# Kernel tuning notes

Hardware: AMD Instinct MI355X
Metric: run time of the kernel (lower is better)

The kernel has to match this reference:

```python
import jax, jax.numpy as jnp
import numpy as np
from jax import lax

V = 10475
J = 55
B = 512
# Kinematic tree: hardcoded chain (parent[i] = i-1), root = 0.
PARENTS = np.concatenate([[-1], np.arange(J - 1)]).astype(np.int32)


def rodrigues(r):
    """Axis-angle (..., 3) -> rotation matrices (..., 3, 3)."""
    angle = jnp.sqrt(jnp.sum(r * r, axis=-1, keepdims=True) + 1e-12)  # (...,1)
    axis = r / angle
    s = jnp.sin(angle)[..., None]
    c = jnp.cos(angle)[..., None]
    kx, ky, kz = axis[..., 0], axis[..., 1], axis[..., 2]
    z = jnp.zeros_like(kx)
    K = jnp.stack([z, -kz, ky, kz, z, -kx, -ky, kx, z], axis=-1).reshape(r.shape[:-1] + (3, 3))
    I = jnp.eye(3, dtype=r.dtype)
    return I + s * K + (1.0 - c) * (K @ K)


def setup_inputs() -> dict:
    key = jax.random.key(0)
    ks = jax.random.split(key, 16)
    inp = {
        'shape': jax.random.normal(ks[0], (1, 10), jnp.float32),
        'body_pose': jax.random.normal(ks[1], (B, 21, 3), jnp.float32) * 0.3,
        'hand_pose': jax.random.normal(ks[2], (B, 30, 3), jnp.float32) * 0.3,
        'head_pose': jax.random.normal(ks[3], (B, 3, 3), jnp.float32) * 0.3,
        'expression': jax.random.normal(ks[4], (B, 10), jnp.float32),
        'pelvis_rotation': jax.random.normal(ks[5], (B, 3), jnp.float32) * 0.3,
        'global_translation': jax.random.normal(ks[6], (B, 3), jnp.float32),
        'v_template': jax.random.normal(ks[7], (V, 3), jnp.float32),
        'shapedirs': jax.random.normal(ks[8], (V, 3, 10), jnp.float32) * 0.01,
        'exprdirs': jax.random.normal(ks[9], (V, 3, 10), jnp.float32) * 0.01,
        'posedirs': jax.random.normal(ks[10], (486, V * 3), jnp.float32) * 0.001,
    }
    w = jax.random.uniform(ks[11], (V, J), jnp.float32)
    inp['lbs_weights'] = w / jnp.sum(w, axis=-1, keepdims=True)
    jr = jax.random.uniform(ks[12], (J, V), jnp.float32)
    inp['J_regressor'] = jr / jnp.sum(jr, axis=-1, keepdims=True)
    inp['hand_mean'] = jax.random.normal(ks[13], (2, 45), jnp.float32) * 0.1
    return inp


def reference(shape, body_pose, hand_pose, head_pose, expression, pelvis_rotation,
              global_translation, v_template, shapedirs, exprdirs, posedirs,
              lbs_weights, J_regressor, hand_mean):
    b = body_pose.shape[0]
    dtype = v_template.dtype

    # 1) shape + expression blendshapes -> (B, V, 3)
    v_shaped = (v_template[None]
                + jnp.einsum('bs,vcs->bvc', shape, shapedirs)
                + jnp.einsum('be,vce->bvc', expression, exprdirs))

    # 2) joint locations (B, J, 3)
    joints = jnp.einsum('jv,bvc->bjc', J_regressor, v_shaped)

    # 3) assemble full pose (B, 55, 3): pelvis | body(21) | head(3) | hands(30)
    hands = hand_pose.reshape(b, 90) + hand_mean.reshape(90)[None]
    full_pose = jnp.concatenate(
        [pelvis_rotation[:, None], body_pose, head_pose, hands.reshape(b, 30, 3)], axis=1)
    rotmats = rodrigues(full_pose)  # (B, J, 3, 3)

    # 4) pose blendshapes
    I3 = jnp.eye(3, dtype=dtype)
    pose_feature = (rotmats[:, 1:] - I3).reshape(b, (J - 1) * 9)  # (B, 486)
    v_posed = v_shaped + (pose_feature @ posedirs).reshape(b, V, 3)

    # 5) local joint transforms (B, J, 4, 4)
    rel_joints = joints.at[:, 1:].add(-joints[:, PARENTS[1:]])
    top = jnp.concatenate([rotmats, rel_joints[..., None]], axis=-1)  # (B,J,3,4)
    bottom = jnp.broadcast_to(
        jnp.array([0., 0., 0., 1.], dtype=dtype), (b, J, 1, 4))
    T_local = jnp.concatenate([top, bottom], axis=-2)

    # 6) compose along kinematic chain (parent[i] = i-1 -> scan)
    def step(G_prev, T_i):
        G = G_prev @ T_i  # (B,4,4)
        return G, G
    G0 = T_local[:, 0]
    _, Gs = lax.scan(step, G0, jnp.swapaxes(T_local[:, 1:], 0, 1))
    G = jnp.concatenate([G0[:, None], jnp.swapaxes(Gs, 0, 1)], axis=1)  # (B,J,4,4)

    # 7) remove rest-pose joint locations: A = G * inv(rest)
    A = G.at[..., :3, 3].add(-jnp.einsum('bjrc,bjc->bjr', G[..., :3, :3], joints))

    # 8) linear blend skinning
    T = jnp.einsum('vj,bjrc->bvrc', lbs_weights, A)  # (B,V,4,4)
    verts = jnp.einsum('bvrc,bvc->bvr', T[..., :3, :3], v_posed) + T[..., :3, 3]

    # 9) ground plane + global translation
    y_offset = -jnp.min(v_template[:, 1])
    verts = verts.at[..., 1].add(y_offset)
    verts = verts + global_translation[:, None]
    return verts
```

## Files before the change

kernel.cpp:

```cpp
#include <hip/hip_runtime.h>
#include <hip/hip_bf16.h>


typedef _Float16 f16;
typedef f16  f16x8 __attribute__((ext_vector_type(8)));
typedef f16  f16x4 __attribute__((ext_vector_type(4)));
typedef float f32x4 __attribute__((ext_vector_type(4)));

#define VN    10475
#define JN    55
#define BN    512
#define VC3   31425
#define NPAD  31488
#define VPADV 10496

#define SD_F  0
#define JS_F  31425
#define JE_F  31590
#define Y_F   33240
#define PFH_BYTE  (160*1024)
#define AH_BYTE   (768*1024)
#define VPH_BYTE  (2*1024*1024)
#define LWT_BYTE  (34*1024*1024)

__global__ void k_sdirs(const float* __restrict__ vt, const float* __restrict__ shapedirs,
                        const float* __restrict__ shape, float* __restrict__ ws)
{
    int i = blockIdx.x * 256 + threadIdx.x;
    if (i >= VC3) return;
    float acc = vt[i];
    const float* sd = shapedirs + (size_t)i * 10;
    #pragma unroll
    for (int s = 0; s < 10; ++s) acc += shape[s] * sd[s];
    ws[SD_F + i] = acc;
}

__global__ void k_ymin(const float* __restrict__ vt, float* __restrict__ ws)
{
    __shared__ float red[256];
    int tid = threadIdx.x;
    float m = 3.0e38f;
    for (int v = tid; v < VN; v += 256) m = fminf(m, vt[v*3 + 1]);
    red[tid] = m;
    __syncthreads();
    for (int s = 128; s > 0; s >>= 1) {
        if (tid < s) red[tid] = fminf(red[tid], red[tid + s]);
        __syncthreads();
    }
    if (tid == 0) ws[Y_F] = -red[0];
}

__global__ void k_jreg(const float* __restrict__ jr, const float* __restrict__ exprdirs,
                       float* __restrict__ ws)
{
    int j = blockIdx.x / 3, c = blockIdx.x % 3;
    int tid = threadIdx.x;
    const float* sdir = ws + SD_F;
    float acc[11];
    #pragma unroll
    for (int i = 0; i < 11; ++i) acc[i] = 0.f;
    for (int v = tid; v < VN; v += 256) {
        float w = jr[(size_t)j * VN + v];
        acc[10] += w * sdir[v*3 + c];
        const float* ed = exprdirs + (size_t)(v*3 + c) * 10;
        #pragma unroll
        for (int e = 0; e < 10; ++e) acc[e] += w * ed[e];
    }
    __shared__ float red[256];
    for (int i = 0; i < 11; ++i) {
        red[tid] = acc[i];
        __syncthreads();
        for (int s = 128; s > 0; s >>= 1) {
            if (tid < s) red[tid] += red[tid + s];
            __syncthreads();
        }
        if (tid == 0) {
            if (i == 10) ws[JS_F + j*3 + c] = red[0];
            else         ws[JE_F + (j*3 + c)*10 + i] = red[0];
        }
        __syncthreads();
    }
}

__global__ void k_lwT(const float* __restrict__ lw, f16* __restrict__ lwT)
{
    int t = threadIdx.x;
    int v  = blockIdx.x * 64 + (t >> 2);
    int jg = (t & 3) * 16;
    f16 tmp[16];
    #pragma unroll
    for (int jj = 0; jj < 16; ++jj) {
        int j = jg + jj;
        tmp[jj] = (f16)((v < VN && j < JN) ? lw[(size_t)v*JN + j] : 0.f);
    }
    int vt = v >> 4, lv = v & 15;
    int ks = jg >> 5, q0 = (jg >> 3) & 3;
    *(f16x8*)&lwT[(size_t)vt*1024 + ks*512 + (q0*16 + lv)*8]     = *(f16x8*)&tmp[0];
    *(f16x8*)&lwT[(size_t)vt*1024 + ks*512 + ((q0+1)*16 + lv)*8] = *(f16x8*)&tmp[8];
}

__global__ void k_batch(const float* __restrict__ body, const float* __restrict__ hand,
                        const float* __restrict__ head, const float* __restrict__ expr,
                        const float* __restrict__ pelvis, const float* __restrict__ hand_mean,
                        const float* __restrict__ ws, f16* __restrict__ PFH,
                        f16* __restrict__ AH)
{
    int b = blockIdx.x, tid = threadIdx.x;
    __shared__ float rot[JN][9];
    __shared__ float jnt[JN][3];

    f16* AHb = AH + (size_t)b * 1024;
    #pragma unroll
    for (int i = 0; i < 16; ++i) AHb[tid + i*64] = (f16)0.f;

    if (tid < JN) {
        int j = tid;
        float r0, r1, r2;
        if (j == 0) {
            r0 = pelvis[b*3+0]; r1 = pelvis[b*3+1]; r2 = pelvis[b*3+2];
        } else if (j <= 21) {
            int o = b*63 + (j-1)*3;
            r0 = body[o]; r1 = body[o+1]; r2 = body[o+2];
        } else if (j <= 24) {
            int o = b*9 + (j-22)*3;
            r0 = head[o]; r1 = head[o+1]; r2 = head[o+2];
        } else {
            int h = (j-25)*3;
            r0 = hand[b*90+h+0] + hand_mean[h+0];
            r1 = hand[b*90+h+1] + hand_mean[h+1];
            r2 = hand[b*90+h+2] + hand_mean[h+2];
        }
        float a2  = r0*r0 + r1*r1 + r2*r2 + 1e-12f;
        float ang = sqrtf(a2);
        float inv = 1.0f / ang;
        float kx = r0*inv, ky = r1*inv, kz = r2*inv;
        float s = sinf(ang), c = cosf(ang), ic = 1.0f - c;
        rot[j][0] = c + ic*kx*kx;    rot[j][1] = ic*kx*ky - s*kz; rot[j][2] = ic*kx*kz + s*ky;
        rot[j][3] = ic*kx*ky + s*kz; rot[j][4] = c + ic*ky*ky;    rot[j][5] = ic*ky*kz - s*kx;
        rot[j][6] = ic*kx*kz - s*ky; rot[j][7] = ic*ky*kz + s*kx; rot[j][8] = c + ic*kz*kz;
        #pragma unroll
        for (int cc = 0; cc < 3; ++cc) {
            float acc = ws[JS_F + j*3 + cc];
            #pragma unroll
            for (int e = 0; e < 10; ++e)
                acc += expr[b*10 + e] * ws[JE_F + (j*3 + cc)*10 + e];
            jnt[j][cc] = acc;
        }
    }
    __syncthreads();

    #pragma unroll
    for (int i = 0; i < 8; ++i) {
        int k = tid + i*64;
        float val = 0.f;
        if (k < 486) {
            int jj = k/9 + 1, ii = k%9;
            float d = (ii == 0 || ii == 4 || ii == 8) ? 1.0f : 0.0f;
            val = rot[jj][ii] - d;
        } else if (k < 496) {
            val = expr[b*10 + (k-486)];
        }
        PFH[(size_t)((b>>4)*16 + (k>>5))*512 + (((k>>3)&3)*16 + (b&15))*8 + (k&7)] = (f16)val;
    }

    int r = tid >> 2, cc = tid & 3;
    float g = 0.f;
    if (tid < 12) g = (cc < 3) ? rot[0][r*3 + cc] : jnt[0][r];
    for (int j = 0; j < JN; ++j) {
        if (j > 0) {
            float g0 = __shfl(g, r*4+0), g1 = __shfl(g, r*4+1);
            float g2 = __shfl(g, r*4+2), g3 = __shfl(g, r*4+3);
            if (cc < 3) g = g0*rot[j][cc] + g1*rot[j][3+cc] + g2*rot[j][6+cc];
            else        g = g0*(jnt[j][0]-jnt[j-1][0]) + g1*(jnt[j][1]-jnt[j-1][1])
                          + g2*(jnt[j][2]-jnt[j-1][2]) + g3;
        }
        float h0 = __shfl(g, r*4+0), h1 = __shfl(g, r*4+1), h2 = __shfl(g, r*4+2);
        float aval = g;
        if (cc == 3) aval = g - (h0*jnt[j][0] + h1*jnt[j][1] + h2*jnt[j][2]);
        if (tid < 12)
            AHb[(j>>5)*512 + (((j>>3)&3)*16 + tid)*8 + (j&7)] = (f16)aval;
    }
}

#define BTS 520
#define LTS 72
__global__ __launch_bounds__(256, 2) void k_pose(
    const float* __restrict__ pd, const float* __restrict__ ed,
    const float* __restrict__ ws, const f16* __restrict__ PFH,
    f16* __restrict__ VPH2)
{
    __shared__ f16 SH[BN*LTS];
    __shared__ float SDl[64];
    const int t = threadIdx.x;
    const int n0 = blockIdx.x * 64;
    const int w = t >> 6, lane = t & 63, l = lane & 15, q = lane >> 4;
    f16* Bt = SH;

    {
        const int krow = t & 15, f = t >> 4;
        const int nb = n0 + f*4;
        #pragma unroll 4
        for (int it = 0; it < 32; ++it) {
            int k = krow + it*16;
            float4 vv = make_float4(0.f, 0.f, 0.f, 0.f);
            if (k < 486) {
                if (nb + 3 < VC3) vv = *(const float4*)(pd + (size_t)k*VC3 + nb);
                else {
                    float* pv = (float*)&vv;
                    for (int e = 0; e < 4; ++e)
                        if (nb + e < VC3) pv[e] = pd[(size_t)k*VC3 + nb + e];
                }
            } else if (k < 496) {
                float* pv = (float*)&vv;
                for (int e = 0; e < 4; ++e)
                    if (nb + e < VC3) pv[e] = ed[(size_t)(nb + e)*10 + (k - 486)];
            }
            int c = f*4;
            Bt[(c+0)*BTS + k] = (f16)vv.x;
            Bt[(c+1)*BTS + k] = (f16)vv.y;
            Bt[(c+2)*BTS + k] = (f16)vv.z;
            Bt[(c+3)*BTS + k] = (f16)vv.w;
        }
    }
    if (t < 64) { int n = n0 + t; SDl[t] = (n < VC3) ? ws[SD_F + n] : 0.f; }
    __syncthreads();

    f32x4 acc[4][8];
    #pragma unroll
    for (int i = 0; i < 4; ++i)
        #pragma unroll
        for (int j = 0; j < 8; ++j) acc[i][j] = (f32x4)0.f;

    for (int kc = 0; kc < 16; ++kc) {
        f16x8 af[4], bf[8];
        #pragma unroll
        for (int mt = 0; mt < 4; ++mt)
            af[mt] = *(const f16x8*)&Bt[(mt*16 + l)*BTS + kc*32 + q*8];
        #pragma unroll
        for (int nt = 0; nt < 8; ++nt)
            bf[nt] = *(const f16x8*)&PFH[(size_t)((w*8 + nt)*16 + kc)*512 + lane*8];
        #pragma unroll
        for (int mt = 0; mt < 4; ++mt)
            #pragma unroll
            for (int nt = 0; nt < 8; ++nt)
                acc[mt][nt] = __builtin_amdgcn_mfma_f32_16x16x32_f16(af[mt], bf[nt], acc[mt][nt], 0, 0, 0);
    }

    __syncthreads();
    f16* L = SH;
    #pragma unroll
    for (int mt = 0; mt < 4; ++mt)
        #pragma unroll
        for (int nt = 0; nt < 8; ++nt) {
            int b = w*128 + nt*16 + l;
            f16 pack[4];
            #pragma unroll
            for (int i = 0; i < 4; ++i) {
                int c = mt*16 + q*4 + i;
                pack[i] = (f16)(acc[mt][nt][i] + SDl[c]);
            }
            *(f16x4*)&L[b*LTS + mt*16 + q*4] = *(f16x4*)&pack[0];
        }
    __syncthreads();
    {
        const int c4 = (t & 15) * 4, bq = t >> 4;
        #pragma unroll 4
        for (int it = 0; it < 32; ++it) {
            int b = bq + 16*it;
            *(f16x4*)&VPH2[(size_t)b*NPAD + n0 + c4] = *(const f16x4*)&L[b*LTS + c4];
        }
    }
}

__global__ __launch_bounds__(256, 8) void k_lbs(
    const float* __restrict__ gt, const float* __restrict__ ws,
    const f16* __restrict__ AH, const f16* __restrict__ lwT,
    const f16* __restrict__ VPH2, float* __restrict__ out)
{
    __shared__ f16 LV[8*192];
    const int t = threadIdx.x;
    const int v0 = blockIdx.x * 64;
    const int bbase = blockIdx.y * 8;
    const int w = t >> 6, lane = t & 63, l = lane & 15, q = lane >> 4;

    if (t < 192) {
        int bl = t / 24, c8 = t % 24;
        *(f16x8*)&LV[bl*192 + c8*8] =
            *(const f16x8*)&VPH2[(size_t)(bbase + bl)*NPAD + v0*3 + c8*8];
    }
    __syncthreads();

    f32x4 acc[2][4];
    #pragma unroll
    for (int i = 0; i < 2; ++i)
        #pragma unroll
        for (int j = 0; j < 4; ++j) acc[i][j] = (f32x4)0.f;

    #pragma unroll
    for (int ks = 0; ks < 2; ++ks) {
        f16x8 af[2], bf[4];
        #pragma unroll
        for (int nt = 0; nt < 4; ++nt)
            bf[nt] = *(const f16x8*)&lwT[(size_t)(blockIdx.x*4 + nt)*1024 + ks*512 + lane*8];
        #pragma unroll
        for (int mt = 0; mt < 2; ++mt)
            af[mt] = *(const f16x8*)&AH[(size_t)(bbase + w*2 + mt)*1024 + ks*512 + lane*8];
        #pragma unroll
        for (int mt = 0; mt < 2; ++mt)
            #pragma unroll
            for (int nt = 0; nt < 4; ++nt)
                acc[mt][nt] = __builtin_amdgcn_mfma_f32_16x16x32_f16(af[mt], bf[nt], acc[mt][nt], 0, 0, 0);
    }

    float yoff = ws[Y_F];
    #pragma unroll
    for (int mt = 0; mt < 2; ++mt) {
        int b = bbase + w*2 + mt;
        float add = (q < 3) ? gt[b*3 + q] + (q == 1 ? yoff : 0.f) : 0.f;
        const f16* vrow = &LV[(w*2 + mt)*192];
        #pragma unroll
        for (int nt = 0; nt < 4; ++nt) {
            int v = v0 + nt*16 + l;
            if (q < 3 && v < VN) {
                int o = (nt*16 + l)*3;
                float vx = (float)vrow[o], vy = (float)vrow[o+1], vz = (float)vrow[o+2];
                f32x4 T = acc[mt][nt];
                out[((size_t)b*VN + v)*3 + q] = T[0]*vx + T[1]*vy + T[2]*vz + T[3] + add;
            }
        }
    }
}

extern "C" void kernel_launch(void* const* d_in, const int* in_sizes, int n_in,
                              void* d_out, int out_size, void* d_ws, size_t ws_size,
                              hipStream_t stream)
{
    const float* shape  = (const float*)d_in[0];
    const float* body   = (const float*)d_in[1];
    const float* hand   = (const float*)d_in[2];
    const float* head   = (const float*)d_in[3];
    const float* expr   = (const float*)d_in[4];
    const float* pelvis = (const float*)d_in[5];
    const float* gtrans = (const float*)d_in[6];
    const float* vt     = (const float*)d_in[7];
    const float* shdirs = (const float*)d_in[8];
    const float* exdirs = (const float*)d_in[9];
    const float* pdirs  = (const float*)d_in[10];
    const float* lbsw   = (const float*)d_in[11];
    const float* jreg   = (const float*)d_in[12];
    const float* hmean  = (const float*)d_in[13];
    float* wsf  = (float*)d_ws;
    f16*   PFH  = (f16*)((char*)d_ws + PFH_BYTE);
    f16*   AH   = (f16*)((char*)d_ws + AH_BYTE);
    f16*   VPH2 = (f16*)((char*)d_ws + VPH_BYTE);
    f16*   lwT  = (f16*)((char*)d_ws + LWT_BYTE);
    float* out  = (float*)d_out;

    hipLaunchKernelGGL(k_sdirs, dim3((VC3 + 255)/256), dim3(256), 0, stream,
                       vt, shdirs, shape, wsf);
    hipLaunchKernelGGL(k_ymin,  dim3(1),    dim3(256), 0, stream, vt, wsf);
    hipLaunchKernelGGL(k_jreg,  dim3(JN*3), dim3(256), 0, stream, jreg, exdirs, wsf);
    hipLaunchKernelGGL(k_lwT,   dim3(VPADV/64), dim3(256), 0, stream, lbsw, lwT);
    hipLaunchKernelGGL(k_batch, dim3(BN),   dim3(64),  0, stream,
                       body, hand, head, expr, pelvis, hmean, wsf, PFH, AH);
    hipLaunchKernelGGL(k_pose,  dim3(NPAD/64), dim3(256), 0, stream,
                       pdirs, exdirs, wsf, PFH, VPH2);
    hipLaunchKernelGGL(k_lbs,   dim3(VPADV/64, 8192/128), dim3(256), 0, stream,
                       gtrans, wsf, AH, lwT, VPH2, out);
}
```

Baseline: 267.6 us.

## Fuse prep kernels into one launch and coalesce LBS output stores via LDS

Merges the shapedirs, y-min, lbs-weight transpose and joint-regressor kernels into a single block-indexed prep kernel. The joint-regressor branch now recomputes the shaped template inline, which removes its dependence on the shapedirs output and lets all four parts run concurrently. k_lbs now stages its outputs in shared memory and writes them back as contiguous per-batch rows, replacing the scattered strided stores. k_pose also hoists an SD load earlier and raises one unroll factor. In exchange, the joint-regressor blocks redo the shapedirs arithmetic, and k_lbs uses more LDS, which may reduce occupancy.

```diff
diff --git a/kernel.cpp b/kernel.cpp
--- a/kernel.cpp
+++ b/kernel.cpp
@@ -23,80 +23,85 @@
 #define VPH_BYTE  (2*1024*1024)
 #define LWT_BYTE  (34*1024*1024)
 
-__global__ void k_sdirs(const float* __restrict__ vt, const float* __restrict__ shapedirs,
-                        const float* __restrict__ shape, float* __restrict__ ws)
-{
-    int i = blockIdx.x * 256 + threadIdx.x;
-    if (i >= VC3) return;
-    float acc = vt[i];
-    const float* sd = shapedirs + (size_t)i * 10;
-    #pragma unroll
-    for (int s = 0; s < 10; ++s) acc += shape[s] * sd[s];
-    ws[SD_F + i] = acc;
-}
-
-__global__ void k_ymin(const float* __restrict__ vt, float* __restrict__ ws)
+#define NB_SD   123
+#define NB_LWT  164
+#define NB_JREG 165
+#define NB_PREP (NB_SD + 1 + NB_LWT + NB_JREG)
+
+__global__ __launch_bounds__(256) void k_prep(
+    const float* __restrict__ vt, const float* __restrict__ shapedirs,
+    const float* __restrict__ shape, const float* __restrict__ lw,
+    const float* __restrict__ jr, const float* __restrict__ exprdirs,
+    float* __restrict__ ws, f16* __restrict__ lwT)
 {
     __shared__ float red[256];
-    int tid = threadIdx.x;
-    float m = 3.0e38f;
-    for (int v = tid; v < VN; v += 256) m = fminf(m, vt[v*3 + 1]);
-    red[tid] = m;
-    __syncthreads();
-    for (int s = 128; s > 0; s >>= 1) {
-        if (tid < s) red[tid] = fminf(red[tid], red[tid + s]);
-        __syncthreads();
-    }
-    if (tid == 0) ws[Y_F] = -red[0];
-}
-
-__global__ void k_jreg(const float* __restrict__ jr, const float* __restrict__ exprdirs,
-                       float* __restrict__ ws)
-{
-    int j = blockIdx.x / 3, c = blockIdx.x % 3;
-    int tid = threadIdx.x;
-    const float* sdir = ws + SD_F;
-    float acc[11];
-    #pragma unroll
-    for (int i = 0; i < 11; ++i) acc[i] = 0.f;
-    for (int v = tid; v < VN; v += 256) {
-        float w = jr[(size_t)j * VN + v];
-        acc[10] += w * sdir[v*3 + c];
-        const float* ed = exprdirs + (size_t)(v*3 + c) * 10;
-        #pragma unroll
-        for (int e = 0; e < 10; ++e) acc[e] += w * ed[e];
-    }
-    __shared__ float red[256];
-    for (int i = 0; i < 11; ++i) {
-        red[tid] = acc[i];
+    const int bb  = blockIdx.x;
+    const int tid = threadIdx.x;
+
+    if (bb < NB_SD) {
+        int i = bb * 256 + tid;
+        if (i < VC3) {
+            float acc = vt[i];
+            const float* sd = shapedirs + (size_t)i * 10;
+            #pragma unroll
+            for (int s = 0; s < 10; ++s) acc += shape[s] * sd[s];
+            ws[SD_F + i] = acc;
+        }
+    } else if (bb == NB_SD) {
+        float m = 3.0e38f;
+        for (int v = tid; v < VN; v += 256) m = fminf(m, vt[v*3 + 1]);
+        red[tid] = m;
         __syncthreads();
         for (int s = 128; s > 0; s >>= 1) {
-            if (tid < s) red[tid] += red[tid + s];
+            if (tid < s) red[tid] = fminf(red[tid], red[tid + s]);
             __syncthreads();
         }
-        if (tid == 0) {
-            if (i == 10) ws[JS_F + j*3 + c] = red[0];
-            else         ws[JE_F + (j*3 + c)*10 + i] = red[0];
-        }
-        __syncthreads();
-    }
-}
-
-__global__ void k_lwT(const float* __restrict__ lw, f16* __restrict__ lwT)
-{
-    int t = threadIdx.x;
-    int v  = blockIdx.x * 64 + (t >> 2);
-    int jg = (t & 3) * 16;
-    f16 tmp[16];
-    #pragma unroll
-    for (int jj = 0; jj < 16; ++jj) {
-        int j = jg + jj;
-        tmp[jj] = (f16)((v < VN && j < JN) ? lw[(size_t)v*JN + j] : 0.f);
-    }
-    int vt = v >> 4, lv = v & 15;
-    int ks = jg >> 5, q0 = (jg >> 3) & 3;
-    *(f16x8*)&lwT[(size_t)vt*1024 + ks*512 + (q0*16 + lv)*8]     = *(f16x8*)&tmp[0];
-    *(f16x8*)&lwT[(size_t)vt*1024 + ks*512 + ((q0+1)*16 + lv)*8] = *(f16x8*)&tmp[8];
+        if (tid == 0) ws[Y_F] = -red[0];
+    } else if (bb < NB_SD + 1 + NB_LWT) {
+        int bx = bb - (NB_SD + 1);
+        int v  = bx * 64 + (tid >> 2);
+        int jg = (tid & 3) * 16;
+        f16 tmp[16];
+        #pragma unroll
+        for (int jj = 0; jj < 16; ++jj) {
+            int j = jg + jj;
+            tmp[jj] = (f16)((v < VN && j < JN) ? lw[(size_t)v*JN + j] : 0.f);
+        }
+        int vtile = v >> 4, lv = v & 15;
+        int ks = jg >> 5, q0 = (jg >> 3) & 3;
+        *(f16x8*)&lwT[(size_t)vtile*1024 + ks*512 + (q0*16 + lv)*8]     = *(f16x8*)&tmp[0];
+        *(f16x8*)&lwT[(size_t)vtile*1024 + ks*512 + ((q0+1)*16 + lv)*8] = *(f16x8*)&tmp[8];
+    } else {
+        int jb = bb - (NB_SD + 1 + NB_LWT);
+        int j = jb / 3, c = jb % 3;
+        float acc[11];
+        #pragma unroll
+        for (int i = 0; i < 11; ++i) acc[i] = 0.f;
+        for (int v = tid; v < VN; v += 256) {
+            float w = jr[(size_t)j * VN + v];
+            float sv = vt[v*3 + c];
+            const float* sd = shapedirs + (size_t)(v*3 + c) * 10;
+            #pragma unroll
+            for (int s = 0; s < 10; ++s) sv += shape[s] * sd[s];
+            acc[10] += w * sv;
+            const float* ed = exprdirs + (size_t)(v*3 + c) * 10;
+            #pragma unroll
+            for (int e = 0; e < 10; ++e) acc[e] += w * ed[e];
+        }
+        for (int i = 0; i < 11; ++i) {
+            red[tid] = acc[i];
+            __syncthreads();
+            for (int s = 128; s > 0; s >>= 1) {
+                if (tid < s) red[tid] += red[tid + s];
+                __syncthreads();
+            }
+            if (tid == 0) {
+                if (i == 10) ws[JS_F + j*3 + c] = red[0];
+                else         ws[JE_F + (j*3 + c)*10 + i] = red[0];
+            }
+            __syncthreads();
+        }
+    }
 }
 
 __global__ void k_batch(const float* __restrict__ body, const float* __restrict__ hand,
@@ -196,10 +201,12 @@
     const int w = t >> 6, lane = t & 63, l = lane & 15, q = lane >> 4;
     f16* Bt = SH;
 
+    if (t < 64) { int n = n0 + t; SDl[t] = (n < VC3) ? ws[SD_F + n] : 0.f; }
+
     {
         const int krow = t & 15, f = t >> 4;
         const int nb = n0 + f*4;
-        #pragma unroll 4
+        #pragma unroll 8
         for (int it = 0; it < 32; ++it) {
             int k = krow + it*16;
             float4 vv = make_float4(0.f, 0.f, 0.f, 0.f);
@@ -222,7 +229,6 @@
             Bt[(c+3)*BTS + k] = (f16)vv.w;
         }
     }
-    if (t < 64) { int n = n0 + t; SDl[t] = (n < VC3) ? ws[SD_F + n] : 0.f; }
     __syncthreads();
 
     f32x4 acc[4][8];
@@ -277,7 +283,8 @@
     const f16* __restrict__ AH, const f16* __restrict__ lwT,
     const f16* __restrict__ VPH2, float* __restrict__ out)
 {
-    __shared__ f16 LV[8*192];
+    __shared__ f16   LV[8*192];
+    __shared__ float OUTS[8*192];
     const int t = threadIdx.x;
     const int v0 = blockIdx.x * 64;
     const int bbase = blockIdx.y * 8;
@@ -315,19 +322,28 @@
     float yoff = ws[Y_F];
     #pragma unroll
     for (int mt = 0; mt < 2; ++mt) {
-        int b = bbase + w*2 + mt;
-        float add = (q < 3) ? gt[b*3 + q] + (q == 1 ? yoff : 0.f) : 0.f;
-        const f16* vrow = &LV[(w*2 + mt)*192];
+        int bl = w*2 + mt;
+        float add = 0.f;
+        if (q < 3) add = gt[(bbase + bl)*3 + q] + (q == 1 ? yoff : 0.f);
+        const f16* vrow = &LV[bl*192];
         #pragma unroll
         for (int nt = 0; nt < 4; ++nt) {
-            int v = v0 + nt*16 + l;
-            if (q < 3 && v < VN) {
+            if (q < 3) {
                 int o = (nt*16 + l)*3;
                 float vx = (float)vrow[o], vy = (float)vrow[o+1], vz = (float)vrow[o+2];
                 f32x4 T = acc[mt][nt];
-                out[((size_t)b*VN + v)*3 + q] = T[0]*vx + T[1]*vy + T[2]*vz + T[3] + add;
-            }
-        }
+                OUTS[bl*192 + o + q] = T[0]*vx + T[1]*vy + T[2]*vz + T[3] + add;
+            }
+        }
+    }
+    __syncthreads();
+    #pragma unroll
+    for (int pass = 0; pass < 6; ++pass) {
+        int idx = pass*256 + t;
+        int bl  = idx / 192;
+        int c   = idx - bl*192;
+        if (v0*3 + c < VC3)
+            out[(size_t)(bbase + bl)*VC3 + v0*3 + c] = OUTS[idx];
     }
 }
 
@@ -356,11 +372,8 @@
     f16*   lwT  = (f16*)((char*)d_ws + LWT_BYTE);
     float* out  = (float*)d_out;
 
-    hipLaunchKernelGGL(k_sdirs, dim3((VC3 + 255)/256), dim3(256), 0, stream,
-                       vt, shdirs, shape, wsf);
-    hipLaunchKernelGGL(k_ymin,  dim3(1),    dim3(256), 0, stream, vt, wsf);
-    hipLaunchKernelGGL(k_jreg,  dim3(JN*3), dim3(256), 0, stream, jreg, exdirs, wsf);
-    hipLaunchKernelGGL(k_lwT,   dim3(VPADV/64), dim3(256), 0, stream, lbsw, lwT);
+    hipLaunchKernelGGL(k_prep,  dim3(NB_PREP), dim3(256), 0, stream,
+                       vt, shdirs, shape, lbsw, jreg, exdirs, wsf, lwT);
     hipLaunchKernelGGL(k_batch, dim3(BN),   dim3(64),  0, stream,
                        body, hand, head, expr, pelvis, hmean, wsf, PFH, AH);
     hipLaunchKernelGGL(k_pose,  dim3(NPAD/64), dim3(256), 0, stream,
```

New measurement: 246.3 us. 8.0% less time.
